# Performance work log

Hardware: AMD Instinct MI355X
Metric: run time of the kernel (lower is better)

The kernel has to match this reference:

```python
import jax, jax.numpy as jnp
import numpy as np

# AdaptiveSoftmax.forward (fairseq), no adaptive_inputs, dropout=0 (eval-equivalent).
# cutoff after __init__ appends vocab_size: [10000, 30000, 50000]
CUTOFF = (10000, 30000, 50000)


def setup_inputs() -> dict:
    key = jax.random.key(0)
    ks = jax.random.split(key, 7)
    B, T, D = 2, 2048, 1024
    head_dim = CUTOFF[0] + (len(CUTOFF) - 1)  # 10002
    d0 = int(D // 4.0 ** 1)  # 256
    d1 = int(D // 4.0 ** 2)  # 64
    inp = {
        "input": jax.random.normal(ks[0], (B, T, D), jnp.float32),
        "target": jax.random.randint(ks[1], (B, T), 0, CUTOFF[-1], jnp.int32),
        # xavier-ish scaled params
        "head_w": jax.random.normal(ks[2], (head_dim, D), jnp.float32) * 0.02,
        "proj0_w": jax.random.normal(ks[3], (d0, D), jnp.float32) * 0.04,
        "out0_w": jax.random.normal(ks[4], (CUTOFF[1] - CUTOFF[0], d0), jnp.float32) * 0.02,
        "proj1_w": jax.random.normal(ks[5], (d1, D), jnp.float32) * 0.06,
        "out1_w": jax.random.normal(ks[6], (CUTOFF[2] - CUTOFF[1], d1), jnp.float32) * 0.02,
    }
    return inp


def reference(input, target, head_w, proj0_w, out0_w, proj1_w, out1_w):
    c0, c1, c2 = CUTOFF
    D = input.shape[-1]
    h = input.reshape(-1, D)            # [N, D] (dropout p=0 -> identity)
    t = target.reshape(-1)              # [N]

    # band membership masks (adapt_target routing)
    m0 = (t >= c0) & (t < c1)
    m1 = (t >= c1) & (t < c2)

    # new_target[0]: tail tokens remapped to class slots c0+i
    new_t_head = jnp.where(m0, c0, jnp.where(m1, c0 + 1, t))
    # per-band relative targets (0 for rows not in the band; original returns
    # ragged gathered targets -- here dense+masked equivalent)
    new_t0 = jnp.where(m0, t - c0, 0)
    new_t1 = jnp.where(m1, t - c1, 0)

    # head: Linear(D -> c0 + n_tails, bias=False)
    head_out = jnp.einsum('nd,vd->nv', h, head_w)  # [N, 10002]

    # tails: proj (D->dim) then out (dim->band_size); original applies only to
    # gathered band rows -- dense version masked to zero outside the band
    # computes the same values on band rows.
    tail0 = jnp.einsum('nk,vk->nv', jnp.einsum('nd,kd->nk', h, proj0_w), out0_w)
    tail0 = tail0 * m0[:, None].astype(tail0.dtype)  # [N, 20000]
    tail1 = jnp.einsum('nk,vk->nv', jnp.einsum('nd,kd->nk', h, proj1_w), out1_w)
    tail1 = tail1 * m1[:, None].astype(tail1.dtype)  # [N, 20000]

    return (head_out, tail0, tail1, new_t_head, new_t0, new_t1)
```

## Files before the change

### kernel.cpp

```cpp
#include <hip/hip_runtime.h>

#define C0 10000
#define C1 30000
#define C2 50000

typedef __attribute__((ext_vector_type(8))) short short8;
typedef __attribute__((ext_vector_type(8))) unsigned short ushort8;
typedef __attribute__((ext_vector_type(4))) float f32x4;

__device__ __forceinline__ unsigned short f2bf(float f) {
    unsigned int u = __float_as_uint(f);
    u += 0x7FFF + ((u >> 16) & 1);
    return (unsigned short)(u >> 16);
}

#define SZ_IN    (4096 * 1024)
#define OFF_IN   0
#define HW_ROWSP 10240
#define SZ_HW    (HW_ROWSP * 1024)
#define REAL_HW  (10002 * 1024)
#define OFF_HW   (OFF_IN + SZ_IN)
#define OFF_PJ   (OFF_HW + SZ_HW)
#define SZ_PJ    (512 * 1024)
#define PJ_P0    (256 * 1024)
#define PJ_P1    (64 * 1024)
#define O_ROWSP  20224
#define SZ_O0    (O_ROWSP * 256)
#define REAL_O0  (20000 * 256)
#define OFF_O0   (OFF_PJ + SZ_PJ)
#define SZ_O1    (O_ROWSP * 64)
#define REAL_O1  (20000 * 64)
#define OFF_O1   (OFF_O0 + SZ_O0)
#define CVT_TOTAL (OFF_O1 + SZ_O1)
#define OFF_PP0C CVT_TOTAL
#define SZ_PP0C  (4096 * 256)
#define OFF_PP1C (OFF_PP0C + SZ_PP0C)
#define SZ_PP1C  (4096 * 64)
#define OFF_IDX  (OFF_PP1C + SZ_PP1C)

__global__ __launch_bounds__(256) void convert_kernel(
    const float* __restrict__ in,  const float* __restrict__ hw,
    const float* __restrict__ p0w, const float* __restrict__ o0w,
    const float* __restrict__ p1w, const float* __restrict__ o1w,
    unsigned short* __restrict__ ws,
    const int* __restrict__ target,
    float* __restrict__ o3, float* __restrict__ o4, float* __restrict__ o5,
    int* __restrict__ idx0, int* __restrict__ idx1, int* __restrict__ cnts)
{
    if (blockIdx.x == 0) {
        __shared__ int wsum0[4], wsum1[4];
        __shared__ int base0s, base1s;
        const int tt = threadIdx.x, lane = tt & 63, wv = tt >> 6;
        if (tt == 0) { base0s = 0; base1s = 0; }
        __syncthreads();
        for (int r = 0; r < 16; r++) {
            int i2 = r * 256 + tt;
            int tg = target[i2];
            bool p0 = (tg >= C0) && (tg < C1);
            bool p1 = (tg >= C1) && (tg < C2);
            unsigned long long b0 = __ballot(p0);
            unsigned long long b1 = __ballot(p1);
            int pre0 = __popcll(b0 & ((1ull << lane) - 1));
            int pre1 = __popcll(b1 & ((1ull << lane) - 1));
            if (lane == 0) { wsum0[wv] = __popcll(b0); wsum1[wv] = __popcll(b1); }
            __syncthreads();
            int woff0 = base0s, woff1 = base1s;
            for (int k = 0; k < wv; k++) { woff0 += wsum0[k]; woff1 += wsum1[k]; }
            if (p0) idx0[woff0 + pre0] = i2;
            if (p1) idx1[woff1 + pre1] = i2;
            __syncthreads();
            if (tt == 0)
                for (int k = 0; k < 4; k++) { base0s += wsum0[k]; base1s += wsum1[k]; }
            __syncthreads();
        }
        for (int j = base0s + tt; j < 4096; j += 256) idx0[j] = 0;
        for (int j = base1s + tt; j < 4096; j += 256) idx1[j] = 0;
        if (tt == 0) { cnts[0] = base0s; cnts[1] = base1s; }
    }

    long long tid = (long long)blockIdx.x * blockDim.x + threadIdx.x;
    if (tid < 4096) {
        int tg = target[tid];
        bool m0 = (tg >= C0) && (tg < C1);
        bool m1 = (tg >= C1) && (tg < C2);
        o3[tid] = (float)(m0 ? C0 : (m1 ? (C0 + 1) : tg));
        o4[tid] = (float)(m0 ? (tg - C0) : 0);
        o5[tid] = (float)(m1 ? (tg - C1) : 0);
    }
    long long i = tid * 8;
    if (i >= CVT_TOTAL) return;
    const float* src;
    long long rel, real;
    if (i < OFF_HW)                      { src = in;  rel = i - OFF_IN;            real = SZ_IN;   }
    else if (i < OFF_PJ)                 { src = hw;  rel = i - OFF_HW;            real = REAL_HW; }
    else if (i < OFF_PJ + PJ_P0)         { src = p0w; rel = i - OFF_PJ;            real = PJ_P0;   }
    else if (i < OFF_PJ + PJ_P0 + PJ_P1) { src = p1w; rel = i - (OFF_PJ + PJ_P0);  real = PJ_P1;   }
    else if (i < OFF_O0)                 { src = p1w; rel = 1;                     real = 0;       }
    else if (i < OFF_O1)                 { src = o0w; rel = i - OFF_O0;            real = REAL_O0; }
    else                                 { src = o1w; rel = i - OFF_O1;            real = REAL_O1; }
    ushort8 o;
    if (rel < real) {
        float4 v0 = *(const float4*)(src + rel);
        float4 v1 = *(const float4*)(src + rel + 4);
        o[0] = f2bf(v0.x); o[1] = f2bf(v0.y); o[2] = f2bf(v0.z); o[3] = f2bf(v0.w);
        o[4] = f2bf(v1.x); o[5] = f2bf(v1.y); o[6] = f2bf(v1.z); o[7] = f2bf(v1.w);
    } else {
        o = (ushort8)0;
    }
    *(ushort8*)(ws + i) = o;
}

#define BM 128
#define BN 128
#define BK 64

__global__ __launch_bounds__(256) void proj_gather(
    const unsigned short* __restrict__ A,
    const unsigned short* __restrict__ pjw,
    unsigned short* __restrict__ pp0c, unsigned short* __restrict__ pp1c,
    const int* __restrict__ idx0, const int* __restrict__ idx1,
    const int* __restrict__ cnts)
{
    const int band = blockIdx.z;
    if (band == 1 && blockIdx.x > 0) return;
    const int* idx = band ? idx1 : idx0;
    const int cnt = cnts[band];
    const int mBase = blockIdx.y * BM;
    if (mBase >= cnt) return;
    const unsigned short* B = pjw + (band ? (size_t)PJ_P0 : 0);
    const int Nn = band ? 64 : 256;
    unsigned short* Cb = band ? pp1c : pp0c;
    const int K = 1024;

    __shared__ unsigned short As[BM * BK];
    __shared__ unsigned short Bs[BN * BK];

    const int t    = threadIdx.x;
    const int lane = t & 63;
    const int w    = t >> 6;
    const int wr   = w >> 1;
    const int wc   = w & 1;
    const int nBase = blockIdx.x * BN;
    const int srow = lane >> 3;
    const int scol = (lane & 7) * 8;

    int rowsIdx[4];
    #pragma unroll
    for (int c = 0; c < 4; c++)
        rowsIdx[c] = idx[mBase + w * 32 + c * 8 + srow];

    f32x4 acc[4][4] = {};

    for (int k0 = 0; k0 < K; k0 += BK) {
        #pragma unroll
        for (int c = 0; c < 4; c++) {
            const int rbase = w * 32 + c * 8;
            const unsigned short* ga = A + (size_t)rowsIdx[c] * K + k0 + scol;
            __builtin_amdgcn_global_load_lds(
                (const __attribute__((address_space(1))) void*)ga,
                (__attribute__((address_space(3))) void*)&As[rbase * BK], 16, 0, 0);
            const unsigned short* gb = B + (size_t)(nBase + rbase + srow) * K + k0 + scol;
            __builtin_amdgcn_global_load_lds(
                (const __attribute__((address_space(1))) void*)gb,
                (__attribute__((address_space(3))) void*)&Bs[rbase * BK], 16, 0, 0);
        }
        __syncthreads();

        #pragma unroll
        for (int kk = 0; kk < BK / 32; kk++) {
            const int kOff = kk * 32 + (lane >> 4) * 8;
            short8 a4[4], b4[4];
            #pragma unroll
            for (int m = 0; m < 4; m++)
                a4[m] = *(const short8*)(&As[(wr * 64 + m * 16 + (lane & 15)) * BK + kOff]);
            #pragma unroll
            for (int n = 0; n < 4; n++)
                b4[n] = *(const short8*)(&Bs[(wc * 64 + n * 16 + (lane & 15)) * BK + kOff]);
            #pragma unroll
            for (int m = 0; m < 4; m++)
                #pragma unroll
                for (int n = 0; n < 4; n++)
                    acc[m][n] = __builtin_amdgcn_mfma_f32_16x16x32_bf16(
                        a4[m], b4[n], acc[m][n], 0, 0, 0);
        }
        __syncthreads();
    }

    #pragma unroll
    for (int m = 0; m < 4; m++)
        #pragma unroll
        for (int i = 0; i < 4; i++) {
            int grow = mBase + wr * 64 + m * 16 + (lane >> 4) * 4 + i;
            #pragma unroll
            for (int n = 0; n < 4; n++) {
                int gcol = nBase + wc * 64 + n * 16 + (lane & 15);
                if (gcol < Nn)
                    Cb[(size_t)grow * Nn + gcol] = f2bf(acc[m][n][i]);
            }
        }
}


__device__ __forceinline__ short8 ldsw(const unsigned short* base, int row, int chunk) {
    int slot = chunk ^ (row & 7);
    return *(const short8*)(base + row * 64 + slot * 8);
}

#define STG(dstElemOff, srcPtr)                                                \
  __builtin_amdgcn_global_load_lds(                                            \
      (const __attribute__((address_space(1))) void*)(srcPtr),                 \
      (__attribute__((address_space(3))) void*)(lds + (dstElemOff)), 16, 0, 0);

#define STAGE_A(bf, h, kofs) {                                                 \
    STG((bf)*32768 + (h)*8192 + (w * 8) * 64,        pA[h] + (kofs));          \
    STG((bf)*32768 + (h)*8192 + (64 + w * 8) * 64,   pA[h] + (size_t)64 * K + (kofs)); }
#define STAGE_B(bf, h, kofs) {                                                 \
    STG((bf)*32768 + 16384 + (h)*8192 + (w * 8) * 64,      pB[h] + (kofs));    \
    STG((bf)*32768 + 16384 + (h)*8192 + (64 + w * 8) * 64, pB[h] + (size_t)64 * K + (kofs)); }

#define VM4()  asm volatile("s_waitcnt vmcnt(4)" ::: "memory")
#define BARF() { __builtin_amdgcn_s_barrier(); asm volatile("" ::: "memory"); }

#define NB_FUSED 3200
#define TAIL_SLOTS 2528

__global__ __launch_bounds__(512) void fused_kernel(
    const unsigned short* __restrict__ in_bf, const unsigned short* __restrict__ hw_bf,
    const unsigned short* __restrict__ pp0c,  const unsigned short* __restrict__ pp1c,
    const unsigned short* __restrict__ o0w,   const unsigned short* __restrict__ o1w,
    float* __restrict__ head_out, float* __restrict__ tail0, float* __restrict__ tail1,
    const int* __restrict__ idx0, const int* __restrict__ idx1,
    const int* __restrict__ cnts, const int* __restrict__ target)
{
    __shared__ unsigned short lds[65536];

    const int L    = blockIdx.x;
    const int t    = threadIdx.x;
    const int lane = t & 63;
    const int w    = t >> 6;
    const int wm   = w >> 2;
    const int wn   = w & 3;
    const int lr   = lane & 15;
    const int lq   = lane >> 4;
    const int lr3  = lane >> 3;
    const int swzc = ((lane & 7) ^ lr3) * 8;

    const unsigned short *A = nullptr, *B = nullptr;
    float* Cp = nullptr;
    const int* idx = nullptr;
    int K = 0, NT = 0, Nn = 0, Mlimit = 0, mBase = 0, nBase = 0;
    bool live = false;

    if (L % 5 == 0) {
        int h = L / 5;
        int swz = (h & 7) * 80 + (h >> 3);
        nBase = (swz >> 4) * 256;
        mBase = (swz & 15) * 256;
        A = in_bf; B = hw_bf; Cp = head_out;
        K = 1024; NT = 16; Nn = 10002; Mlimit = 4096;
        live = true;
    } else {
        int s = L - L / 5 - 1;
        if (s < TAIL_SLOTS) {
            int band = s / 1264;
            int r    = s % 1264;
            nBase = (r / 16) * 256;
            mBase = (r % 16) * 256;
            if (band == 0) { A = pp0c; B = o0w; Cp = tail0; idx = idx0; K = 256; NT = 4; }
            else           { A = pp1c; B = o1w; Cp = tail1; idx = idx1; K = 64;  NT = 1; }
            Nn = 20000;
            Mlimit = cnts[band];
            live = (mBase < Mlimit);
        }
    }

    if (live) {
        const unsigned short* pA[2];
        const unsigned short* pB[2];
        #pragma unroll
        for (int h = 0; h < 2; h++) {
            pA[h] = A + (size_t)(mBase + h * 128 + w * 8 + lr3) * K + swzc;
            pB[h] = B + (size_t)(nBase + h * 128 + w * 8 + lr3) * K + swzc;
        }

        f32x4 acc[8][4] = {};
        short8 af[4][2], bf0[2][2], bf1[2][2];

        STAGE_A(0, 0, 0); STAGE_B(0, 0, 0); STAGE_B(0, 1, 0); STAGE_A(0, 1, 0);

        for (int kt = 0; kt < NT; ++kt) {
            const int cb = kt & 1, nb2 = cb ^ 1;
            const int kofs = (kt + 1) * 64;
            const unsigned short* Ab0 = lds + cb * 32768;
            const unsigned short* Ab1 = Ab0 + 8192;
            const unsigned short* Bb0 = Ab0 + 16384;
            const unsigned short* Bb1 = Ab0 + 24576;

            VM4(); BARF();
            #pragma unroll
            for (int m = 0; m < 4; m++)
                #pragma unroll
                for (int ks = 0; ks < 2; ks++)
                    af[m][ks] = ldsw(Ab0, wm * 64 + m * 16 + lr, ks * 4 + lq);
            #pragma unroll
            for (int n = 0; n < 2; n++)
                #pragma unroll
                for (int ks = 0; ks < 2; ks++)
                    bf0[n][ks] = ldsw(Bb0, wn * 32 + n * 16 + lr, ks * 4 + lq);
            STAGE_A(nb2, 0, kofs);
            __builtin_amdgcn_s_setprio(1);
            #pragma unroll
            for (int m = 0; m < 4; m++)
                #pragma unroll
                for (int n = 0; n < 2; n++)
                    #pragma unroll
                    for (int ks = 0; ks < 2; ks++)
                        acc[m][n] = __builtin_amdgcn_mfma_f32_16x16x32_bf16(
                            af[m][ks], bf0[n][ks], acc[m][n], 0, 0, 0);
            __builtin_amdgcn_s_setprio(0);

            VM4(); BARF();
            #pragma unroll
            for (int n = 0; n < 2; n++)
                #pragma unroll
                for (int ks = 0; ks < 2; ks++)
                    bf1[n][ks] = ldsw(Bb1, wn * 32 + n * 16 + lr, ks * 4 + lq);
            STAGE_B(nb2, 0, kofs);
            __builtin_amdgcn_s_setprio(1);
            #pragma unroll
            for (int m = 0; m < 4; m++)
                #pragma unroll
                for (int n = 0; n < 2; n++)
                    #pragma unroll
                    for (int ks = 0; ks < 2; ks++)
                        acc[m][2 + n] = __builtin_amdgcn_mfma_f32_16x16x32_bf16(
                            af[m][ks], bf1[n][ks], acc[m][2 + n], 0, 0, 0);
            __builtin_amdgcn_s_setprio(0);

            VM4(); BARF();
            #pragma unroll
            for (int m = 0; m < 4; m++)
                #pragma unroll
                for (int ks = 0; ks < 2; ks++)
                    af[m][ks] = ldsw(Ab1, wm * 64 + m * 16 + lr, ks * 4 + lq);
            STAGE_B(nb2, 1, kofs);
            __builtin_amdgcn_s_setprio(1);
            #pragma unroll
            for (int m = 0; m < 4; m++)
                #pragma unroll
                for (int n = 0; n < 2; n++)
                    #pragma unroll
                    for (int ks = 0; ks < 2; ks++)
                        acc[4 + m][2 + n] = __builtin_amdgcn_mfma_f32_16x16x32_bf16(
                            af[m][ks], bf1[n][ks], acc[4 + m][2 + n], 0, 0, 0);
            __builtin_amdgcn_s_setprio(0);

            BARF();
            STAGE_A(nb2, 1, kofs);
            __builtin_amdgcn_s_setprio(1);
            #pragma unroll
            for (int m = 0; m < 4; m++)
                #pragma unroll
                for (int n = 0; n < 2; n++)
                    #pragma unroll
                    for (int ks = 0; ks < 2; ks++)
                        acc[4 + m][n] = __builtin_amdgcn_mfma_f32_16x16x32_bf16(
                            af[m][ks], bf0[n][ks], acc[4 + m][n], 0, 0, 0);
            __builtin_amdgcn_s_setprio(0);
        }

        #pragma unroll
        for (int m = 0; m < 8; m++) {
            const int growb = mBase + (m >> 2) * 128 + wm * 64 + (m & 3) * 16 + lq * 4;
            #pragma unroll
            for (int i = 0; i < 4; i++) {
                int grow = growb + i;
                if (grow < Mlimit) {
                    int gr = idx ? idx[grow] : grow;
                    #pragma unroll
                    for (int n = 0; n < 4; n++) {
                        int gcol = nBase + (n >> 1) * 128 + wn * 32 + (n & 1) * 16 + lr;
                        if (gcol < Nn)
                            Cp[(size_t)gr * Nn + gcol] = acc[m][n][i];
                    }
                }
            }
        }
    }

    for (int j = L; j < 8192; j += NB_FUSED) {
        int row   = j >> 1;
        int which = j & 1;
        int tg = target[row];
        bool in = which ? (tg >= C1 && tg < C2) : (tg >= C0 && tg < C1);
        if (!in) {
            float4* dst = (float4*)((which ? tail1 : tail0) + (size_t)row * 20000);
            float4 z = {0.f, 0.f, 0.f, 0.f};
            for (int q = t; q < 5000; q += 512) dst[q] = z;
        }
    }
}

extern "C" void kernel_launch(void* const* d_in, const int* in_sizes, int n_in,
                              void* d_out, int out_size, void* d_ws, size_t ws_size,
                              hipStream_t stream)
{
    const float* input   = (const float*)d_in[0];
    const int*   target  = (const int*)  d_in[1];
    const float* head_w  = (const float*)d_in[2];
    const float* proj0_w = (const float*)d_in[3];
    const float* out0_w  = (const float*)d_in[4];
    const float* proj1_w = (const float*)d_in[5];
    const float* out1_w  = (const float*)d_in[6];

    const int N = 4096;

    float* out      = (float*)d_out;
    float* head_out = out;
    float* tail0    = head_out + (size_t)N * 10002;
    float* tail1    = tail0 + (size_t)N * 20000;
    float* o3       = tail1 + (size_t)N * 20000;
    float* o4       = o3 + N;
    float* o5       = o4 + N;

    unsigned short* ws = (unsigned short*)d_ws;
    unsigned short* in_bf  = ws + OFF_IN;
    unsigned short* hw_bf  = ws + OFF_HW;
    unsigned short* pjw_bf = ws + OFF_PJ;
    unsigned short* o0w_bf = ws + OFF_O0;
    unsigned short* o1w_bf = ws + OFF_O1;
    unsigned short* pp0c   = ws + OFF_PP0C;
    unsigned short* pp1c   = ws + OFF_PP1C;
    int* idx0 = (int*)(ws + OFF_IDX);
    int* idx1 = idx0 + 4096;
    int* cnts = idx1 + 4096;

    convert_kernel<<<dim3((CVT_TOTAL / 8 + 255) / 256), dim3(256), 0, stream>>>(
        input, head_w, proj0_w, out0_w, proj1_w, out1_w, ws, target, o3, o4, o5,
        idx0, idx1, cnts);

    proj_gather<<<dim3(2, N / BM, 2), dim3(256), 0, stream>>>(
        in_bf, pjw_bf, pp0c, pp1c, idx0, idx1, cnts);

    fused_kernel<<<dim3(NB_FUSED), dim3(512), 0, stream>>>(
        in_bf, hw_bf, pp0c, pp1c, o0w_bf, o1w_bf,
        head_out, tail0, tail1, idx0, idx1, cnts, target);
}
```

Before: 316.9 us.

## Fuse gathered projection GEMM into convert kernel to drop a launch

The separate proj_gather kernel is merged into the conversion kernel as 96 extra blocks. Each of these blocks recomputes its band's compaction on its own, reads fp32 input and projection weights straight from global memory, converts them to bf16 on the fly, and runs the small MFMA GEMM. This removes one kernel launch and the dependency on the converted bf16 workspace, so the projection can overlap the bulk conversion. The cost is a redundant prefix scan over 4096 targets in every projection block, fp32 loads that are twice as wide, and register-staged LDS writes instead of direct global-to-LDS loads.

```diff
diff --git a/kernel.cpp b/kernel.cpp
--- a/kernel.cpp
+++ b/kernel.cpp
@@ -38,20 +38,137 @@
 #define SZ_PP1C  (4096 * 64)
 #define OFF_IDX  (OFF_PP1C + SZ_PP1C)
 
-__global__ __launch_bounds__(256) void convert_kernel(
+#define NB_PROJ 96
+#define NB_CVT  ((CVT_TOTAL / 8 + 255) / 256)
+
+__global__ __launch_bounds__(256) void convert_proj_kernel(
     const float* __restrict__ in,  const float* __restrict__ hw,
     const float* __restrict__ p0w, const float* __restrict__ o0w,
     const float* __restrict__ p1w, const float* __restrict__ o1w,
     unsigned short* __restrict__ ws,
     const int* __restrict__ target,
     float* __restrict__ o3, float* __restrict__ o4, float* __restrict__ o5,
+    unsigned short* __restrict__ pp0c, unsigned short* __restrict__ pp1c,
     int* __restrict__ idx0, int* __restrict__ idx1, int* __restrict__ cnts)
 {
-    if (blockIdx.x == 0) {
-        __shared__ int wsum0[4], wsum1[4];
-        __shared__ int base0s, base1s;
-        const int tt = threadIdx.x, lane = tt & 63, wv = tt >> 6;
-        if (tt == 0) { base0s = 0; base1s = 0; }
+    __shared__ int lidx[128];
+    __shared__ int wsumP0[4], wsumP1[4];
+    __shared__ int baseP0, baseP1;
+    __shared__ unsigned short As[128 * 64];
+    __shared__ unsigned short Bs[128 * 64];
+
+    const int tt = threadIdx.x, lane = tt & 63, wv = tt >> 6;
+
+    if (blockIdx.x < NB_PROJ) {
+        const int pid  = blockIdx.x;
+        const int band = (pid >= 64) ? 1 : 0;
+        const int r0   = band ? pid - 64 : pid;
+        const int my   = band ? r0 : (r0 >> 1);
+        const int nb   = band ? 0 : (r0 & 1);
+        const int mBase = my * 128;
+        const int nBase = nb * 128;
+        const int realB = band ? 64 : 256;
+        const float* wsrc = band ? p1w : p0w;
+        unsigned short* Cb = band ? pp1c : pp0c;
+        const int Nn = band ? 64 : 256;
+
+        for (int j = tt; j < 128; j += 256) lidx[j] = 0;
+        if (tt == 0) baseP0 = 0;
+        __syncthreads();
+        for (int rr = 0; rr < 16; rr++) {
+            int i2 = rr * 256 + tt;
+            int tg = target[i2];
+            bool p = band ? (tg >= C1 && tg < C2) : (tg >= C0 && tg < C1);
+            unsigned long long b = __ballot(p);
+            int pre = __popcll(b & ((1ull << lane) - 1));
+            if (lane == 0) wsumP0[wv] = __popcll(b);
+            __syncthreads();
+            int woff = baseP0;
+            for (int k = 0; k < wv; k++) woff += wsumP0[k];
+            int pos = woff + pre;
+            if (p && pos >= mBase && pos < mBase + 128) lidx[pos - mBase] = i2;
+            __syncthreads();
+            if (tt == 0) for (int k = 0; k < 4; k++) baseP0 += wsumP0[k];
+            __syncthreads();
+        }
+        const int cnt = baseP0;
+        if (mBase >= cnt) return;
+
+        const int w  = tt >> 6;
+        const int wr = w >> 1, wc = w & 1;
+        const int rowL = tt >> 3;
+        const int colL = (tt & 7) * 8;
+
+        f32x4 acc[4][4] = {};
+
+        for (int k0 = 0; k0 < 1024; k0 += 64) {
+            #pragma unroll
+            for (int p = 0; p < 4; p++) {
+                int row = p * 32 + rowL;
+                const float* s = in + (size_t)lidx[row] * 1024 + k0 + colL;
+                float4 v0 = *(const float4*)s;
+                float4 v1 = *(const float4*)(s + 4);
+                ushort8 o;
+                o[0]=f2bf(v0.x); o[1]=f2bf(v0.y); o[2]=f2bf(v0.z); o[3]=f2bf(v0.w);
+                o[4]=f2bf(v1.x); o[5]=f2bf(v1.y); o[6]=f2bf(v1.z); o[7]=f2bf(v1.w);
+                *(ushort8*)(&As[row * 64 + colL]) = o;
+            }
+            #pragma unroll
+            for (int p = 0; p < 4; p++) {
+                int row = p * 32 + rowL;
+                int gr = nBase + row;
+                ushort8 o;
+                if (gr < realB) {
+                    const float* s = wsrc + (size_t)gr * 1024 + k0 + colL;
+                    float4 v0 = *(const float4*)s;
+                    float4 v1 = *(const float4*)(s + 4);
+                    o[0]=f2bf(v0.x); o[1]=f2bf(v0.y); o[2]=f2bf(v0.z); o[3]=f2bf(v0.w);
+                    o[4]=f2bf(v1.x); o[5]=f2bf(v1.y); o[6]=f2bf(v1.z); o[7]=f2bf(v1.w);
+                } else {
+                    o = (ushort8)0;
+                }
+                *(ushort8*)(&Bs[row * 64 + colL]) = o;
+            }
+            __syncthreads();
+            #pragma unroll
+            for (int kk = 0; kk < 2; kk++) {
+                const int kOff = kk * 32 + (lane >> 4) * 8;
+                short8 a4[4], b4[4];
+                #pragma unroll
+                for (int m = 0; m < 4; m++)
+                    a4[m] = *(const short8*)(&As[(wr * 64 + m * 16 + (lane & 15)) * 64 + kOff]);
+                #pragma unroll
+                for (int n = 0; n < 4; n++)
+                    b4[n] = *(const short8*)(&Bs[(wc * 64 + n * 16 + (lane & 15)) * 64 + kOff]);
+                #pragma unroll
+                for (int m = 0; m < 4; m++)
+                    #pragma unroll
+                    for (int n = 0; n < 4; n++)
+                        acc[m][n] = __builtin_amdgcn_mfma_f32_16x16x32_bf16(
+                            a4[m], b4[n], acc[m][n], 0, 0, 0);
+            }
+            __syncthreads();
+        }
+
+        #pragma unroll
+        for (int m = 0; m < 4; m++)
+            #pragma unroll
+            for (int i = 0; i < 4; i++) {
+                int grow = mBase + wr * 64 + m * 16 + (lane >> 4) * 4 + i;
+                #pragma unroll
+                for (int n = 0; n < 4; n++) {
+                    int gcol = nBase + wc * 64 + n * 16 + (lane & 15);
+                    if (gcol < Nn)
+                        Cb[(size_t)grow * Nn + gcol] = f2bf(acc[m][n][i]);
+                }
+            }
+        return;
+    }
+
+    const int cb = blockIdx.x - NB_PROJ;
+
+    if (cb == 0) {
+        if (tt == 0) { baseP0 = 0; baseP1 = 0; }
         __syncthreads();
         for (int r = 0; r < 16; r++) {
             int i2 = r * 256 + tt;
@@ -62,23 +179,23 @@
             unsigned long long b1 = __ballot(p1);
             int pre0 = __popcll(b0 & ((1ull << lane) - 1));
             int pre1 = __popcll(b1 & ((1ull << lane) - 1));
-            if (lane == 0) { wsum0[wv] = __popcll(b0); wsum1[wv] = __popcll(b1); }
-            __syncthreads();
-            int woff0 = base0s, woff1 = base1s;
-            for (int k = 0; k < wv; k++) { woff0 += wsum0[k]; woff1 += wsum1[k]; }
+            if (lane == 0) { wsumP0[wv] = __popcll(b0); wsumP1[wv] = __popcll(b1); }
+            __syncthreads();
+            int woff0 = baseP0, woff1 = baseP1;
+            for (int k = 0; k < wv; k++) { woff0 += wsumP0[k]; woff1 += wsumP1[k]; }
             if (p0) idx0[woff0 + pre0] = i2;
             if (p1) idx1[woff1 + pre1] = i2;
             __syncthreads();
             if (tt == 0)
-                for (int k = 0; k < 4; k++) { base0s += wsum0[k]; base1s += wsum1[k]; }
-            __syncthreads();
-        }
-        for (int j = base0s + tt; j < 4096; j += 256) idx0[j] = 0;
-        for (int j = base1s + tt; j < 4096; j += 256) idx1[j] = 0;
-        if (tt == 0) { cnts[0] = base0s; cnts[1] = base1s; }
-    }
-
-    long long tid = (long long)blockIdx.x * blockDim.x + threadIdx.x;
+                for (int k = 0; k < 4; k++) { baseP0 += wsumP0[k]; baseP1 += wsumP1[k]; }
+            __syncthreads();
+        }
+        for (int j = baseP0 + tt; j < 4096; j += 256) idx0[j] = 0;
+        for (int j = baseP1 + tt; j < 4096; j += 256) idx1[j] = 0;
+        if (tt == 0) { cnts[0] = baseP0; cnts[1] = baseP1; }
+    }
+
+    long long tid = (long long)cb * blockDim.x + threadIdx.x;
     if (tid < 4096) {
         int tg = target[tid];
         bool m0 = (tg >= C0) && (tg < C1);
@@ -108,96 +225,6 @@
         o = (ushort8)0;
     }
     *(ushort8*)(ws + i) = o;
-}
-
-#define BM 128
-#define BN 128
-#define BK 64
-
-__global__ __launch_bounds__(256) void proj_gather(
-    const unsigned short* __restrict__ A,
-    const unsigned short* __restrict__ pjw,
-    unsigned short* __restrict__ pp0c, unsigned short* __restrict__ pp1c,
-    const int* __restrict__ idx0, const int* __restrict__ idx1,
-    const int* __restrict__ cnts)
-{
-    const int band = blockIdx.z;
-    if (band == 1 && blockIdx.x > 0) return;
-    const int* idx = band ? idx1 : idx0;
-    const int cnt = cnts[band];
-    const int mBase = blockIdx.y * BM;
-    if (mBase >= cnt) return;
-    const unsigned short* B = pjw + (band ? (size_t)PJ_P0 : 0);
-    const int Nn = band ? 64 : 256;
-    unsigned short* Cb = band ? pp1c : pp0c;
-    const int K = 1024;
-
-    __shared__ unsigned short As[BM * BK];
-    __shared__ unsigned short Bs[BN * BK];
-
-    const int t    = threadIdx.x;
-    const int lane = t & 63;
-    const int w    = t >> 6;
-    const int wr   = w >> 1;
-    const int wc   = w & 1;
-    const int nBase = blockIdx.x * BN;
-    const int srow = lane >> 3;
-    const int scol = (lane & 7) * 8;
-
-    int rowsIdx[4];
-    #pragma unroll
-    for (int c = 0; c < 4; c++)
-        rowsIdx[c] = idx[mBase + w * 32 + c * 8 + srow];
-
-    f32x4 acc[4][4] = {};
-
-    for (int k0 = 0; k0 < K; k0 += BK) {
-        #pragma unroll
-        for (int c = 0; c < 4; c++) {
-            const int rbase = w * 32 + c * 8;
-            const unsigned short* ga = A + (size_t)rowsIdx[c] * K + k0 + scol;
-            __builtin_amdgcn_global_load_lds(
-                (const __attribute__((address_space(1))) void*)ga,
-                (__attribute__((address_space(3))) void*)&As[rbase * BK], 16, 0, 0);
-            const unsigned short* gb = B + (size_t)(nBase + rbase + srow) * K + k0 + scol;
-            __builtin_amdgcn_global_load_lds(
-                (const __attribute__((address_space(1))) void*)gb,
-                (__attribute__((address_space(3))) void*)&Bs[rbase * BK], 16, 0, 0);
-        }
-        __syncthreads();
-
-        #pragma unroll
-        for (int kk = 0; kk < BK / 32; kk++) {
-            const int kOff = kk * 32 + (lane >> 4) * 8;
-            short8 a4[4], b4[4];
-            #pragma unroll
-            for (int m = 0; m < 4; m++)
-                a4[m] = *(const short8*)(&As[(wr * 64 + m * 16 + (lane & 15)) * BK + kOff]);
-            #pragma unroll
-            for (int n = 0; n < 4; n++)
-                b4[n] = *(const short8*)(&Bs[(wc * 64 + n * 16 + (lane & 15)) * BK + kOff]);
-            #pragma unroll
-            for (int m = 0; m < 4; m++)
-                #pragma unroll
-                for (int n = 0; n < 4; n++)
-                    acc[m][n] = __builtin_amdgcn_mfma_f32_16x16x32_bf16(
-                        a4[m], b4[n], acc[m][n], 0, 0, 0);
-        }
-        __syncthreads();
-    }
-
-    #pragma unroll
-    for (int m = 0; m < 4; m++)
-        #pragma unroll
-        for (int i = 0; i < 4; i++) {
-            int grow = mBase + wr * 64 + m * 16 + (lane >> 4) * 4 + i;
-            #pragma unroll
-            for (int n = 0; n < 4; n++) {
-                int gcol = nBase + wc * 64 + n * 16 + (lane & 15);
-                if (gcol < Nn)
-                    Cb[(size_t)grow * Nn + gcol] = f2bf(acc[m][n][i]);
-            }
-        }
 }
 
 
@@ -289,9 +316,9 @@
         STAGE_A(0, 0, 0); STAGE_B(0, 0, 0); STAGE_B(0, 1, 0); STAGE_A(0, 1, 0);
 
         for (int kt = 0; kt < NT; ++kt) {
-            const int cb = kt & 1, nb2 = cb ^ 1;
+            const int cbuf = kt & 1, nb2 = cbuf ^ 1;
             const int kofs = (kt + 1) * 64;
-            const unsigned short* Ab0 = lds + cb * 32768;
+            const unsigned short* Ab0 = lds + cbuf * 32768;
             const unsigned short* Ab1 = Ab0 + 8192;
             const unsigned short* Bb0 = Ab0 + 16384;
             const unsigned short* Bb1 = Ab0 + 24576;
@@ -426,7 +453,6 @@
     unsigned short* ws = (unsigned short*)d_ws;
     unsigned short* in_bf  = ws + OFF_IN;
     unsigned short* hw_bf  = ws + OFF_HW;
-    unsigned short* pjw_bf = ws + OFF_PJ;
     unsigned short* o0w_bf = ws + OFF_O0;
     unsigned short* o1w_bf = ws + OFF_O1;
     unsigned short* pp0c   = ws + OFF_PP0C;
@@ -435,12 +461,9 @@
     int* idx1 = idx0 + 4096;
     int* cnts = idx1 + 4096;
 
-    convert_kernel<<<dim3((CVT_TOTAL / 8 + 255) / 256), dim3(256), 0, stream>>>(
+    convert_proj_kernel<<<dim3(NB_CVT + NB_PROJ), dim3(256), 0, stream>>>(
         input, head_w, proj0_w, out0_w, proj1_w, out1_w, ws, target, o3, o4, o5,
-        idx0, idx1, cnts);
-
-    proj_gather<<<dim3(2, N / BM, 2), dim3(256), 0, stream>>>(
-        in_bf, pjw_bf, pp0c, pp1c, idx0, idx1, cnts);
+        pp0c, pp1c, idx0, idx1, cnts);
 
     fused_kernel<<<dim3(NB_FUSED), dim3(512), 0, stream>>>(
         in_bf, hw_bf, pp0c, pp1c, o0w_bf, o1w_bf,
```

After: 330.2 us. 1.04x slower.

## Replace 256x256 pipelined fused GEMM with 128x128 single-buffered mega kernel

Applied to the files above, without the earlier changes.

Swaps the 512-thread kernel, which used 256x256 tiles, double-buffered swizzled LDS and a hand-interleaved prefetch schedule, for a 256-thread kernel with 128x128 tiles and simple load/sync/compute loops. Head, tail0 and tail1 tiles and the zero-fill rows are interleaved across a much larger grid, with dedicated blocks handling zeroing. Tail padding shrinks to a multiple of 128 rows. The smaller tiles give more blocks and lower per-block LDS use, which may improve occupancy and load balance. In exchange, data reuse per tile is lower, there is no swizzling (possible LDS bank conflicts) and load latency is no longer overlapped with compute.

```diff
diff --git a/kernel.cpp b/kernel.cpp
--- a/kernel.cpp
+++ b/kernel.cpp
@@ -24,7 +24,7 @@
 #define SZ_PJ    (512 * 1024)
 #define PJ_P0    (256 * 1024)
 #define PJ_P1    (64 * 1024)
-#define O_ROWSP  20224
+#define O_ROWSP  20096
 #define SZ_O0    (O_ROWSP * 256)
 #define REAL_O0  (20000 * 256)
 #define OFF_O0   (OFF_PJ + SZ_PJ)
@@ -201,30 +201,12 @@
 }
 
 
-__device__ __forceinline__ short8 ldsw(const unsigned short* base, int row, int chunk) {
-    int slot = chunk ^ (row & 7);
-    return *(const short8*)(base + row * 64 + slot * 8);
-}
-
-#define STG(dstElemOff, srcPtr)                                                \
-  __builtin_amdgcn_global_load_lds(                                            \
-      (const __attribute__((address_space(1))) void*)(srcPtr),                 \
-      (__attribute__((address_space(3))) void*)(lds + (dstElemOff)), 16, 0, 0);
-
-#define STAGE_A(bf, h, kofs) {                                                 \
-    STG((bf)*32768 + (h)*8192 + (w * 8) * 64,        pA[h] + (kofs));          \
-    STG((bf)*32768 + (h)*8192 + (64 + w * 8) * 64,   pA[h] + (size_t)64 * K + (kofs)); }
-#define STAGE_B(bf, h, kofs) {                                                 \
-    STG((bf)*32768 + 16384 + (h)*8192 + (w * 8) * 64,      pB[h] + (kofs));    \
-    STG((bf)*32768 + 16384 + (h)*8192 + (64 + w * 8) * 64, pB[h] + (size_t)64 * K + (kofs)); }
-
-#define VM4()  asm volatile("s_waitcnt vmcnt(4)" ::: "memory")
-#define BARF() { __builtin_amdgcn_s_barrier(); asm volatile("" ::: "memory"); }
-
-#define NB_FUSED 3200
-#define TAIL_SLOTS 2528
-
-__global__ __launch_bounds__(512) void fused_kernel(
+#define HEAD_TILES 2528
+#define TAIL_SL    5024
+#define NGROUPS    4192
+#define MEGA_GRID  (NGROUPS * 5)
+
+__global__ __launch_bounds__(256) void mega128(
     const unsigned short* __restrict__ in_bf, const unsigned short* __restrict__ hw_bf,
     const unsigned short* __restrict__ pp0c,  const unsigned short* __restrict__ pp1c,
     const unsigned short* __restrict__ o0w,   const unsigned short* __restrict__ o1w,
@@ -232,173 +214,113 @@
     const int* __restrict__ idx0, const int* __restrict__ idx1,
     const int* __restrict__ cnts, const int* __restrict__ target)
 {
-    __shared__ unsigned short lds[65536];
-
-    const int L    = blockIdx.x;
-    const int t    = threadIdx.x;
+    __shared__ unsigned short As[BM * BK];
+    __shared__ unsigned short Bs[BN * BK];
+
+    const int L = blockIdx.x;
+    const int G = L / 5;
+    const int r = L % 5;
+    const int t = threadIdx.x;
+
+    if (r >= 3) {
+        int f = G * 2 + (r - 3);
+        if (f >= 8192) return;
+        int row   = f >> 1;
+        int which = f & 1;
+        int tg = target[row];
+        bool in = which ? (tg >= C1 && tg < C2) : (tg >= C0 && tg < C1);
+        if (in) return;
+        float4* dst = (float4*)((which ? tail1 : tail0) + (size_t)row * 20000);
+        float4 z = {0.f, 0.f, 0.f, 0.f};
+        for (int q = t; q < 5000; q += 256) dst[q] = z;
+        return;
+    }
+
+    const int s = G * 3 + r;
+    const unsigned short *A, *B;
+    float* Cp;
+    const int* idx = nullptr;
+    int K, Nn, Mlimit, mBase, nBase;
+
+    if (s < HEAD_TILES) {
+        int by = s % 32, bx = s / 32;
+        A = in_bf; B = hw_bf; Cp = head_out;
+        K = 1024; Nn = 10002; Mlimit = 4096;
+        mBase = by * 128; nBase = bx * 128;
+    } else if (s < HEAD_TILES + TAIL_SL) {
+        int u = s - HEAD_TILES;
+        int my = u % 32, nb = u / 32;
+        A = pp0c; B = o0w; Cp = tail0; idx = idx0;
+        K = 256; Nn = 20000; Mlimit = cnts[0];
+        mBase = my * 128; nBase = nb * 128;
+    } else {
+        int u = s - HEAD_TILES - TAIL_SL;
+        int my = u % 32, nb = u / 32;
+        A = pp1c; B = o1w; Cp = tail1; idx = idx1;
+        K = 64; Nn = 20000; Mlimit = cnts[1];
+        mBase = my * 128; nBase = nb * 128;
+    }
+    if (mBase >= Mlimit) return;
+
     const int lane = t & 63;
     const int w    = t >> 6;
-    const int wm   = w >> 2;
-    const int wn   = w & 3;
-    const int lr   = lane & 15;
-    const int lq   = lane >> 4;
-    const int lr3  = lane >> 3;
-    const int swzc = ((lane & 7) ^ lr3) * 8;
-
-    const unsigned short *A = nullptr, *B = nullptr;
-    float* Cp = nullptr;
-    const int* idx = nullptr;
-    int K = 0, NT = 0, Nn = 0, Mlimit = 0, mBase = 0, nBase = 0;
-    bool live = false;
-
-    if (L % 5 == 0) {
-        int h = L / 5;
-        int swz = (h & 7) * 80 + (h >> 3);
-        nBase = (swz >> 4) * 256;
-        mBase = (swz & 15) * 256;
-        A = in_bf; B = hw_bf; Cp = head_out;
-        K = 1024; NT = 16; Nn = 10002; Mlimit = 4096;
-        live = true;
-    } else {
-        int s = L - L / 5 - 1;
-        if (s < TAIL_SLOTS) {
-            int band = s / 1264;
-            int r    = s % 1264;
-            nBase = (r / 16) * 256;
-            mBase = (r % 16) * 256;
-            if (band == 0) { A = pp0c; B = o0w; Cp = tail0; idx = idx0; K = 256; NT = 4; }
-            else           { A = pp1c; B = o1w; Cp = tail1; idx = idx1; K = 64;  NT = 1; }
-            Nn = 20000;
-            Mlimit = cnts[band];
-            live = (mBase < Mlimit);
-        }
-    }
-
-    if (live) {
-        const unsigned short* pA[2];
-        const unsigned short* pB[2];
-        #pragma unroll
-        for (int h = 0; h < 2; h++) {
-            pA[h] = A + (size_t)(mBase + h * 128 + w * 8 + lr3) * K + swzc;
-            pB[h] = B + (size_t)(nBase + h * 128 + w * 8 + lr3) * K + swzc;
-        }
-
-        f32x4 acc[8][4] = {};
-        short8 af[4][2], bf0[2][2], bf1[2][2];
-
-        STAGE_A(0, 0, 0); STAGE_B(0, 0, 0); STAGE_B(0, 1, 0); STAGE_A(0, 1, 0);
-
-        for (int kt = 0; kt < NT; ++kt) {
-            const int cb = kt & 1, nb2 = cb ^ 1;
-            const int kofs = (kt + 1) * 64;
-            const unsigned short* Ab0 = lds + cb * 32768;
-            const unsigned short* Ab1 = Ab0 + 8192;
-            const unsigned short* Bb0 = Ab0 + 16384;
-            const unsigned short* Bb1 = Ab0 + 24576;
-
-            VM4(); BARF();
+    const int wr   = w >> 1;
+    const int wc   = w & 1;
+    const int srow = lane >> 3;
+    const int scol = (lane & 7) * 8;
+
+    f32x4 acc[4][4] = {};
+
+    for (int k0 = 0; k0 < K; k0 += BK) {
+        #pragma unroll
+        for (int c = 0; c < 4; c++) {
+            const int rbase = w * 32 + c * 8;
+            const unsigned short* ga = A + (size_t)(mBase + rbase + srow) * K + k0 + scol;
+            __builtin_amdgcn_global_load_lds(
+                (const __attribute__((address_space(1))) void*)ga,
+                (__attribute__((address_space(3))) void*)&As[rbase * BK], 16, 0, 0);
+            const unsigned short* gb = B + (size_t)(nBase + rbase + srow) * K + k0 + scol;
+            __builtin_amdgcn_global_load_lds(
+                (const __attribute__((address_space(1))) void*)gb,
+                (__attribute__((address_space(3))) void*)&Bs[rbase * BK], 16, 0, 0);
+        }
+        __syncthreads();
+
+        #pragma unroll
+        for (int kk = 0; kk < BK / 32; kk++) {
+            const int kOff = kk * 32 + (lane >> 4) * 8;
+            short8 a4[4], b4[4];
+            #pragma unroll
+            for (int m = 0; m < 4; m++)
+                a4[m] = *(const short8*)(&As[(wr * 64 + m * 16 + (lane & 15)) * BK + kOff]);
+            #pragma unroll
+            for (int n = 0; n < 4; n++)
+                b4[n] = *(const short8*)(&Bs[(wc * 64 + n * 16 + (lane & 15)) * BK + kOff]);
             #pragma unroll
             for (int m = 0; m < 4; m++)
                 #pragma unroll
-                for (int ks = 0; ks < 2; ks++)
-                    af[m][ks] = ldsw(Ab0, wm * 64 + m * 16 + lr, ks * 4 + lq);
-            #pragma unroll
-            for (int n = 0; n < 2; n++)
+                for (int n = 0; n < 4; n++)
+                    acc[m][n] = __builtin_amdgcn_mfma_f32_16x16x32_bf16(
+                        a4[m], b4[n], acc[m][n], 0, 0, 0);
+        }
+        __syncthreads();
+    }
+
+    #pragma unroll
+    for (int m = 0; m < 4; m++)
+        #pragma unroll
+        for (int i = 0; i < 4; i++) {
+            int grow = mBase + wr * 64 + m * 16 + (lane >> 4) * 4 + i;
+            if (grow < Mlimit) {
+                int gr = idx ? idx[grow] : grow;
                 #pragma unroll
-                for (int ks = 0; ks < 2; ks++)
-                    bf0[n][ks] = ldsw(Bb0, wn * 32 + n * 16 + lr, ks * 4 + lq);
-            STAGE_A(nb2, 0, kofs);
-            __builtin_amdgcn_s_setprio(1);
-            #pragma unroll
-            for (int m = 0; m < 4; m++)
-                #pragma unroll
-                for (int n = 0; n < 2; n++)
-                    #pragma unroll
-                    for (int ks = 0; ks < 2; ks++)
-                        acc[m][n] = __builtin_amdgcn_mfma_f32_16x16x32_bf16(
-                            af[m][ks], bf0[n][ks], acc[m][n], 0, 0, 0);
-            __builtin_amdgcn_s_setprio(0);
-
-            VM4(); BARF();
-            #pragma unroll
-            for (int n = 0; n < 2; n++)
-                #pragma unroll
-                for (int ks = 0; ks < 2; ks++)
-                    bf1[n][ks] = ldsw(Bb1, wn * 32 + n * 16 + lr, ks * 4 + lq);
-            STAGE_B(nb2, 0, kofs);
-            __builtin_amdgcn_s_setprio(1);
-            #pragma unroll
-            for (int m = 0; m < 4; m++)
-                #pragma unroll
-                for (int n = 0; n < 2; n++)
-                    #pragma unroll
-                    for (int ks = 0; ks < 2; ks++)
-                        acc[m][2 + n] = __builtin_amdgcn_mfma_f32_16x16x32_bf16(
-                            af[m][ks], bf1[n][ks], acc[m][2 + n], 0, 0, 0);
-            __builtin_amdgcn_s_setprio(0);
-
-            VM4(); BARF();
-            #pragma unroll
-            for (int m = 0; m < 4; m++)
-                #pragma unroll
-                for (int ks = 0; ks < 2; ks++)
-                    af[m][ks] = ldsw(Ab1, wm * 64 + m * 16 + lr, ks * 4 + lq);
-            STAGE_B(nb2, 1, kofs);
-            __builtin_amdgcn_s_setprio(1);
-            #pragma unroll
-            for (int m = 0; m < 4; m++)
-                #pragma unroll
-                for (int n = 0; n < 2; n++)
-                    #pragma unroll
-                    for (int ks = 0; ks < 2; ks++)
-                        acc[4 + m][2 + n] = __builtin_amdgcn_mfma_f32_16x16x32_bf16(
-                            af[m][ks], bf1[n][ks], acc[4 + m][2 + n], 0, 0, 0);
-            __builtin_amdgcn_s_setprio(0);
-
-            BARF();
-            STAGE_A(nb2, 1, kofs);
-            __builtin_amdgcn_s_setprio(1);
-            #pragma unroll
-            for (int m = 0; m < 4; m++)
-                #pragma unroll
-                for (int n = 0; n < 2; n++)
-                    #pragma unroll
-                    for (int ks = 0; ks < 2; ks++)
-                        acc[4 + m][n] = __builtin_amdgcn_mfma_f32_16x16x32_bf16(
-                            af[m][ks], bf0[n][ks], acc[4 + m][n], 0, 0, 0);
-            __builtin_amdgcn_s_setprio(0);
-        }
-
-        #pragma unroll
-        for (int m = 0; m < 8; m++) {
-            const int growb = mBase + (m >> 2) * 128 + wm * 64 + (m & 3) * 16 + lq * 4;
-            #pragma unroll
-            for (int i = 0; i < 4; i++) {
-                int grow = growb + i;
-                if (grow < Mlimit) {
-                    int gr = idx ? idx[grow] : grow;
-                    #pragma unroll
-                    for (int n = 0; n < 4; n++) {
-                        int gcol = nBase + (n >> 1) * 128 + wn * 32 + (n & 1) * 16 + lr;
-                        if (gcol < Nn)
-                            Cp[(size_t)gr * Nn + gcol] = acc[m][n][i];
-                    }
+                for (int n = 0; n < 4; n++) {
+                    int gcol = nBase + wc * 64 + n * 16 + (lane & 15);
+                    if (gcol < Nn)
+                        Cp[(size_t)gr * Nn + gcol] = acc[m][n][i];
                 }
             }
         }
-    }
-
-    for (int j = L; j < 8192; j += NB_FUSED) {
-        int row   = j >> 1;
-        int which = j & 1;
-        int tg = target[row];
-        bool in = which ? (tg >= C1 && tg < C2) : (tg >= C0 && tg < C1);
-        if (!in) {
-            float4* dst = (float4*)((which ? tail1 : tail0) + (size_t)row * 20000);
-            float4 z = {0.f, 0.f, 0.f, 0.f};
-            for (int q = t; q < 5000; q += 512) dst[q] = z;
-        }
-    }
 }
 
 extern "C" void kernel_launch(void* const* d_in, const int* in_sizes, int n_in,
@@ -442,7 +364,7 @@
     proj_gather<<<dim3(2, N / BM, 2), dim3(256), 0, stream>>>(
         in_bf, pjw_bf, pp0c, pp1c, idx0, idx1, cnts);
 
-    fused_kernel<<<dim3(NB_FUSED), dim3(512), 0, stream>>>(
+    mega128<<<dim3(MEGA_GRID), dim3(256), 0, stream>>>(
         in_bf, hw_bf, pp0c, pp1c, o0w_bf, o1w_bf,
         head_out, tail0, tail1, idx0, idx1, cnts, target);
 }
```

Measured after the change: 428.4 us. 35.2% more time.
